# Kernel tuning notes

Measured on AMD Instinct MI355X. Metric: run time of the kernel, lower is better.

The kernel has to match this reference:

```python
import jax, jax.numpy as jnp
import numpy as np

B, N, D = 2, 2048, 1024
H = 16
DP = D // H          # projection dim per head = 64
SCALE = DP ** 0.5

def setup_inputs() -> dict:
    key = jax.random.key(0)
    ks = jax.random.split(key, 5)
    s_in = 1.0 / np.sqrt(D)
    s_merge = 1.0 / np.sqrt(H * DP)
    x = jax.random.normal(ks[0], (B, N, D), dtype=jnp.float32)
    W_qkv = jax.random.normal(ks[1], (D, 3 * H * DP), dtype=jnp.float32) * s_in
    b_qkv = jnp.zeros((3 * H * DP,), dtype=jnp.float32)
    W_out = jax.random.normal(ks[2], (H * DP, D), dtype=jnp.float32) * s_merge
    b_out = jnp.zeros((D,), dtype=jnp.float32)
    return {"x": x, "W_qkv": W_qkv, "b_qkv": b_qkv, "W_out": W_out, "b_out": b_out}

def reference(x, W_qkv, b_qkv, W_out, b_out):
    # packed QKV projection: (B,N,3*H*DP)
    qkv = jnp.einsum("bnd,de->bne", x, W_qkv) + b_qkv
    # reshape to (B,N,H,3*DP) -> (B,H,N,3*DP), split along last axis
    qkv = qkv.reshape(B, N, H, 3 * DP).transpose(0, 2, 1, 3)
    q, k, v = jnp.split(qkv, 3, axis=-1)                 # each (B,H,N,DP)
    scores = jnp.einsum("bhqd,bhkd->bhqk", q, k) / SCALE  # (B,H,N,N)
    attn = jax.nn.softmax(scores, axis=-1)
    out = jnp.einsum("bhqk,bhkd->bhqd", attn, v)          # (B,H,N,DP)
    out = out.transpose(0, 2, 1, 3).reshape(B, N, H * DP)
    return jnp.einsum("bne,ed->bnd", out, W_out) + b_out
```

## Files before the change

### kernel.cpp

```cpp
#include <hip/hip_runtime.h>
#include <hip/hip_bf16.h>

#define BB 2
#define NN 2048
#define DD 1024
#define HH 16
#define DP 64

typedef __attribute__((ext_vector_type(8))) short short8;
typedef __attribute__((ext_vector_type(4))) short short4v;
typedef __attribute__((ext_vector_type(4))) float float4v;
typedef __attribute__((ext_vector_type(16))) float f32x16;

static __device__ __forceinline__ short f2bf(float f) {
  union { float f; unsigned u; } v; v.f = f;
  unsigned r = v.u + 0x7fffu + ((v.u >> 16) & 1u);
  return (short)(r >> 16);
}

static __device__ __forceinline__ void gload16(const void* g, void* l) {
  __builtin_amdgcn_global_load_lds(
      (const __attribute__((address_space(1))) void*)g,
      (__attribute__((address_space(3))) void*)l, 16, 0, 0);
}

__global__ __launch_bounds__(256) void prep(
    const float* __restrict__ x, short* __restrict__ xb,
    const float* __restrict__ Wqkv, short* __restrict__ wqkt,
    const float* __restrict__ Wout, short* __restrict__ wott) {
  __shared__ short tile[32][33];
  const int b = blockIdx.x, t = threadIdx.x;
  if (b < 4096) {
    int i = (b * 256 + t) * 4;
    float4v f = *(const float4v*)(x + i);
    short4v s;
#pragma unroll
    for (int j = 0; j < 4; ++j) s[j] = f2bf(f[j]);
    *(short4v*)(xb + i) = s;
    return;
  }
  const float* in;  short* out;  int R, C, bx, by;
  if (b < 7168) { int idx = b - 4096; bx = idx % 96; by = idx / 96;
                  in = Wqkv; out = wqkt; R = 1024; C = 3072; }
  else          { int idx = b - 7168; bx = idx % 32; by = idx / 32;
                  in = Wout; out = wott; R = 1024; C = 1024; }
  int c0 = bx * 32, r0 = by * 32;
  int tx = t & 31, ty = t >> 5;
#pragma unroll
  for (int i = 0; i < 32; i += 8)
    tile[ty + i][tx] = f2bf(in[(size_t)(r0 + ty + i) * C + c0 + tx]);
  __syncthreads();
#pragma unroll
  for (int i = 0; i < 32; i += 8)
    out[(size_t)(c0 + ty + i) * R + r0 + tx] = tile[tx][ty + i];
}

__global__ __launch_bounds__(256, 6) void gemm_qkv_mfma(
    const short* __restrict__ A, const short* __restrict__ Bt,
    const float* __restrict__ bias,
    short* __restrict__ Qb, short* __restrict__ Kb, short* __restrict__ Vtb) {
  __shared__ short As[2][64 * 32];
  __shared__ short Bs[2][128 * 32];
  const int K = DD;
  const int t = threadIdx.x;
  const int w = t >> 6, lane = t & 63;
  const int l16 = lane & 15, quad = lane >> 4;
  const int wm = w >> 1, wn = w & 1;
  const int bm0 = blockIdx.y * 64;
  const int bn0 = blockIdx.x * 128;
  const int rA = lane >> 2, cA = lane & 3;
  const short* aRow  = A  + (size_t)(bm0 + w * 16 + rA) * K + cA * 8;
  const short* bRow0 = Bt + (size_t)(bn0 + w * 16 + rA) * K + cA * 8;
  const short* bRow1 = Bt + (size_t)(bn0 + 64 + w * 16 + rA) * K + cA * 8;
  char* AsB = (char*)&As[0][0] + w * 1024;
  char* BsB = (char*)&Bs[0][0] + w * 1024;
  float4v acc[2][4] = {};

  gload16(aRow, AsB);
  gload16(bRow0, BsB);
  gload16(bRow1, BsB + 4096);
  __syncthreads();

  int cur = 0;
  for (int k0 = 0; k0 < K; k0 += 32) {
    if (k0 + 32 < K) {
      const int nxt = cur ^ 1;
      gload16(aRow + k0 + 32, AsB + nxt * 4096);
      gload16(bRow0 + k0 + 32, BsB + nxt * 8192);
      gload16(bRow1 + k0 + 32, BsB + nxt * 8192 + 4096);
    }
    short8 af[2], bf[4];
#pragma unroll
    for (int mb = 0; mb < 2; ++mb)
      af[mb] = *(const short8*)&As[cur][((wm * 32 + mb * 16 + l16) * 4 + quad) * 8];
#pragma unroll
    for (int nb = 0; nb < 4; ++nb)
      bf[nb] = *(const short8*)&Bs[cur][((wn * 64 + nb * 16 + l16) * 4 + quad) * 8];
#pragma unroll
    for (int mb = 0; mb < 2; ++mb)
#pragma unroll
      for (int nb = 0; nb < 4; ++nb)
        acc[mb][nb] = __builtin_amdgcn_mfma_f32_16x16x32_bf16(af[mb], bf[nb],
                                                              acc[mb][nb], 0, 0, 0);
    __syncthreads();
    cur ^= 1;
  }

#pragma unroll
  for (int mb = 0; mb < 2; ++mb)
#pragma unroll
    for (int nb = 0; nb < 4; ++nb)
#pragma unroll
      for (int r = 0; r < 4; ++r) {
        int m = bm0 + wm * 32 + mb * 16 + quad * 4 + r;
        int e = bn0 + wn * 64 + nb * 16 + l16;
        float v = acc[mb][nb][r] + bias[e];
        int b_ = m >> 11;
        int n = m & 2047;
        int h = e / 192;
        int rr = e - h * 192;
        int which = rr >> 6;
        int d = rr & 63;
        if (which == 0)      Qb[((b_ * HH + h) * NN + n) * DP + d] = f2bf(v * 0.125f);
        else if (which == 1) Kb[((b_ * HH + h) * NN + n) * DP + d] = f2bf(v);
        else                 Vtb[((b_ * HH + h) * DP + d) * NN + n] = f2bf(v);
      }
}

__global__ __launch_bounds__(256, 4) void gemm_out_mfma(
    const short* __restrict__ A, const short* __restrict__ Bt,
    const float* __restrict__ bias, float* __restrict__ C) {
  __shared__ short As[2][64 * 32];
  __shared__ short Bs[2][64 * 32];
  const int K = DD;
  const int t = threadIdx.x;
  const int w = t >> 6, lane = t & 63;
  const int l16 = lane & 15, quad = lane >> 4;
  const int wm = w >> 1, wn = w & 1;
  const int bm0 = blockIdx.y * 64;
  const int bn0 = blockIdx.x * 64;
  const int rA = lane >> 2, cA = lane & 3;
  const short* aRow = A  + (size_t)(bm0 + w * 16 + rA) * K + cA * 8;
  const short* bRow = Bt + (size_t)(bn0 + w * 16 + rA) * K + cA * 8;
  char* AsB = (char*)&As[0][0] + w * 1024;
  char* BsB = (char*)&Bs[0][0] + w * 1024;
  float4v acc[2][2] = {};

  gload16(aRow, AsB);
  gload16(bRow, BsB);
  __syncthreads();

  int cur = 0;
  for (int k0 = 0; k0 < K; k0 += 32) {
    if (k0 + 32 < K) {
      const int nxt = cur ^ 1;
      gload16(aRow + k0 + 32, AsB + nxt * 4096);
      gload16(bRow + k0 + 32, BsB + nxt * 4096);
    }
    short8 af[2], bf[2];
#pragma unroll
    for (int mb = 0; mb < 2; ++mb)
      af[mb] = *(const short8*)&As[cur][((wm * 32 + mb * 16 + l16) * 4 + quad) * 8];
#pragma unroll
    for (int nb = 0; nb < 2; ++nb)
      bf[nb] = *(const short8*)&Bs[cur][((wn * 32 + nb * 16 + l16) * 4 + quad) * 8];
#pragma unroll
    for (int mb = 0; mb < 2; ++mb)
#pragma unroll
      for (int nb = 0; nb < 2; ++nb)
        acc[mb][nb] = __builtin_amdgcn_mfma_f32_16x16x32_bf16(af[mb], bf[nb],
                                                              acc[mb][nb], 0, 0, 0);
    __syncthreads();
    cur ^= 1;
  }

#pragma unroll
  for (int mb = 0; mb < 2; ++mb)
#pragma unroll
    for (int nb = 0; nb < 2; ++nb)
#pragma unroll
      for (int r = 0; r < 4; ++r) {
        int m = bm0 + wm * 32 + mb * 16 + quad * 4 + r;
        int e = bn0 + wn * 32 + nb * 16 + l16;
        C[(size_t)m * DD + e] = acc[mb][nb][r] + bias[e];
      }
}

#define FIXMAX 16.0f

__global__ __launch_bounds__(256, 2) void attn_mfma(
    const short* __restrict__ Qb, const short* __restrict__ Kb,
    const short* __restrict__ Vtb, short* __restrict__ Ob) {
  __shared__ short Ks[2][4096];
  __shared__ short Vs[2][4096];

  const int t = threadIdx.x;
  const int w = t >> 6;
  const int lane = t & 63;
  const int l31 = lane & 31;
  const int hi = lane >> 5;
  const int bh = blockIdx.y;
  const int q0 = blockIdx.x * 128 + w * 32;
  const size_t base  = (size_t)bh * NN * DP;
  const size_t baseT = (size_t)bh * DP * NN;

  short8 qf[4];
  {
    const short* qp = Qb + base + (size_t)(q0 + l31) * DP + hi * 8;
#pragma unroll
    for (int c = 0; c < 4; ++c) qf[c] = *(const short8*)(qp + c * 16);
  }

  f32x16 oacc[2] = {};
  float l_loc = 0.f;

  const int sRow = lane >> 3;
  const int sChk = (lane & 7) ^ sRow;
  const short* kSrc = Kb  + base  + (size_t)(w * 16 + sRow) * DP + sChk * 8;
  const short* vSrc = Vtb + baseT + (size_t)(w * 16 + sRow) * NN + sChk * 8;
  char* KsB = (char*)&Ks[0][0] + w * 2048;
  char* VsB = (char*)&Vs[0][0] + w * 2048;

  const int rswz = l31 & 7;
  int chs[4];
#pragma unroll
  for (int c = 0; c < 4; ++c) chs[c] = (((hi + 2 * c) ^ rswz) << 3);

  gload16(kSrc, KsB);
  gload16(kSrc + 8 * DP, KsB + 1024);
  gload16(vSrc, VsB);
  gload16(vSrc + 8 * NN, VsB + 1024);
  __syncthreads();

  for (int tt = 0; tt < NN / 64; ++tt) {
    const int buf = tt & 1;
    if (tt + 1 < NN / 64) {
      const int nxt = buf ^ 1;
      const int k1 = (tt + 1) * 64;
      gload16(kSrc + (size_t)k1 * DP, KsB + nxt * 8192);
      gload16(kSrc + (size_t)k1 * DP + 8 * DP, KsB + nxt * 8192 + 1024);
      gload16(vSrc + k1, VsB + nxt * 8192);
      gload16(vSrc + k1 + 8 * NN, VsB + nxt * 8192 + 1024);
    }
    const short* Kc = &Ks[buf][0];
    const short* Vc = &Vs[buf][0];

    short8 kf[2][4];
#pragma unroll
    for (int nb = 0; nb < 2; ++nb)
#pragma unroll
      for (int c = 0; c < 4; ++c)
        kf[nb][c] = *(const short8*)(Kc + (nb * 32 + l31) * 64 + chs[c]);

    f32x16 sacc[2] = {};
#pragma unroll
    for (int c = 0; c < 4; ++c) {
      sacc[0] = __builtin_amdgcn_mfma_f32_32x32x16_bf16(kf[0][c], qf[c], sacc[0], 0, 0, 0);
      sacc[1] = __builtin_amdgcn_mfma_f32_32x32x16_bf16(kf[1][c], qf[c], sacc[1], 0, 0, 0);
    }

    short8 vf[2][4];
#pragma unroll
    for (int db = 0; db < 2; ++db)
#pragma unroll
      for (int c = 0; c < 4; ++c)
        vf[db][c] = *(const short8*)(Vc + (db * 32 + l31) * 64 + chs[c]);

    short8 pb[4];
#pragma unroll
    for (int b = 0; b < 2; ++b) {
      float pe[16];
#pragma unroll
      for (int r = 0; r < 16; ++r) {
        pe[r] = __expf(sacc[b][r] - FIXMAX);
        l_loc += pe[r];
      }
      unsigned W[8];
#pragma unroll
      for (int j = 0; j < 8; ++j)
        asm("v_cvt_pk_bf16_f32 %0, %1, %2"
            : "=v"(W[j]) : "v"(pe[2 * j]), "v"(pe[2 * j + 1]));
      asm("v_permlane32_swap_b32 %0, %1" : "+v"(W[0]), "+v"(W[2]));
      asm("v_permlane32_swap_b32 %0, %1" : "+v"(W[1]), "+v"(W[3]));
      asm("v_permlane32_swap_b32 %0, %1" : "+v"(W[4]), "+v"(W[6]));
      asm("v_permlane32_swap_b32 %0, %1" : "+v"(W[5]), "+v"(W[7]));
      union { unsigned u[4]; short8 s; } f0, f1;
      f0.u[0] = W[0]; f0.u[1] = W[1]; f0.u[2] = W[2]; f0.u[3] = W[3];
      f1.u[0] = W[4]; f1.u[1] = W[5]; f1.u[2] = W[6]; f1.u[3] = W[7];
      pb[2 * b]     = f0.s;
      pb[2 * b + 1] = f1.s;
    }

#pragma unroll
    for (int c = 0; c < 4; ++c) {
      oacc[0] = __builtin_amdgcn_mfma_f32_32x32x16_bf16(vf[0][c], pb[c], oacc[0], 0, 0, 0);
      oacc[1] = __builtin_amdgcn_mfma_f32_32x32x16_bf16(vf[1][c], pb[c], oacc[1], 0, 0, 0);
    }

    __syncthreads();
  }

  const int b_ = bh >> 4, h = bh & 15;
  const float l_tot = l_loc + __shfl_xor(l_loc, 32);
  const float inv = 1.0f / l_tot;
  const int q = q0 + l31;
  short* orow = Ob + (size_t)(b_ * NN + q) * (HH * DP) + h * DP;
#pragma unroll
  for (int db = 0; db < 2; ++db)
#pragma unroll
    for (int g = 0; g < 4; ++g) {
      short4v s4;
#pragma unroll
      for (int e = 0; e < 4; ++e) s4[e] = f2bf(oacc[db][g * 4 + e] * inv);
      *(short4v*)(orow + db * 32 + g * 8 + hi * 4) = s4;
    }
}

extern "C" void kernel_launch(void* const* d_in, const int* in_sizes, int n_in,
                              void* d_out, int out_size, void* d_ws, size_t ws_size,
                              hipStream_t stream) {
  const float* x    = (const float*)d_in[0];
  const float* Wqkv = (const float*)d_in[1];
  const float* bqkv = (const float*)d_in[2];
  const float* Wout = (const float*)d_in[3];
  const float* bout = (const float*)d_in[4];
  float* out = (float*)d_out;

  const int nQKV = BB * HH * NN * DP;
  const int nX   = BB * NN * DD;
  short* qb   = (short*)d_ws;
  short* kb   = qb + nQKV;
  short* vtb  = kb + nQKV;
  short* ob   = vtb + nQKV;
  short* xb   = ob + nQKV;
  short* wqkt = xb + nX;
  short* wott = wqkt + 3 * HH * DP * DD;

  prep<<<4096 + 3072 + 1024, 256, 0, stream>>>(x, xb, Wqkv, wqkt, Wout, wott);

  gemm_qkv_mfma<<<dim3(3 * HH * DP / 128, BB * NN / 64), 256, 0, stream>>>(
      xb, wqkt, bqkv, qb, kb, vtb);
  attn_mfma<<<dim3(NN / 128, BB * HH), 256, 0, stream>>>(qb, kb, vtb, ob);
  gemm_out_mfma<<<dim3(DD / 64, BB * NN / 64), 256, 0, stream>>>(
      ob, wott, bout, out);
}
```

Before: 209.7 us.

## Enlarge QKV GEMM tile, halve attention block size, use exp2 softmax

The QKV GEMM block tile grows from 64x128 to 128x128, so each wave computes a 64x64 subtile and global loads are reused more, with fewer blocks and more accumulator registers. The attention kernel now runs 2 waves per 128-thread block covering 64 queries, which doubles the number of blocks, and each wave loads more of the K/V tile. The softmax exponent switches from __expf to a native exp2 by folding log2(e) into the Q scale and the fixed max offset. The costs are lower occupancy in the GEMM and more K/V reloads across attention blocks.

```diff
diff --git a/kernel.cpp b/kernel.cpp
--- a/kernel.cpp
+++ b/kernel.cpp
@@ -6,6 +6,8 @@
 #define DD 1024
 #define HH 16
 #define DP 64
+#define QSCALE 0.18033688f
+#define FIX2   23.08312065f
 
 typedef __attribute__((ext_vector_type(8))) short short8;
 typedef __attribute__((ext_vector_type(4))) short short4v;
@@ -55,49 +57,50 @@
     out[(size_t)(c0 + ty + i) * R + r0 + tx] = tile[tx][ty + i];
 }
 
-__global__ __launch_bounds__(256, 6) void gemm_qkv_mfma(
+__global__ __launch_bounds__(256, 3) void gemm_qkv_mfma(
     const short* __restrict__ A, const short* __restrict__ Bt,
     const float* __restrict__ bias,
     short* __restrict__ Qb, short* __restrict__ Kb, short* __restrict__ Vtb) {
-  __shared__ short As[2][64 * 32];
+  __shared__ short As[2][128 * 32];
   __shared__ short Bs[2][128 * 32];
   const int K = DD;
   const int t = threadIdx.x;
   const int w = t >> 6, lane = t & 63;
   const int l16 = lane & 15, quad = lane >> 4;
   const int wm = w >> 1, wn = w & 1;
-  const int bm0 = blockIdx.y * 64;
+  const int bm0 = blockIdx.y * 128;
   const int bn0 = blockIdx.x * 128;
   const int rA = lane >> 2, cA = lane & 3;
-  const short* aRow  = A  + (size_t)(bm0 + w * 16 + rA) * K + cA * 8;
-  const short* bRow0 = Bt + (size_t)(bn0 + w * 16 + rA) * K + cA * 8;
-  const short* bRow1 = Bt + (size_t)(bn0 + 64 + w * 16 + rA) * K + cA * 8;
-  char* AsB = (char*)&As[0][0] + w * 1024;
-  char* BsB = (char*)&Bs[0][0] + w * 1024;
-  float4v acc[2][4] = {};
+  const short* aRow = A  + (size_t)(bm0 + w * 32 + rA) * K + cA * 8;
+  const short* bRow = Bt + (size_t)(bn0 + w * 32 + rA) * K + cA * 8;
+  char* AsB = (char*)&As[0][0] + w * 2048;
+  char* BsB = (char*)&Bs[0][0] + w * 2048;
+  float4v acc[4][4] = {};
 
   gload16(aRow, AsB);
-  gload16(bRow0, BsB);
-  gload16(bRow1, BsB + 4096);
+  gload16(aRow + 16 * K, AsB + 1024);
+  gload16(bRow, BsB);
+  gload16(bRow + 16 * K, BsB + 1024);
   __syncthreads();
 
   int cur = 0;
   for (int k0 = 0; k0 < K; k0 += 32) {
     if (k0 + 32 < K) {
       const int nxt = cur ^ 1;
-      gload16(aRow + k0 + 32, AsB + nxt * 4096);
-      gload16(bRow0 + k0 + 32, BsB + nxt * 8192);
-      gload16(bRow1 + k0 + 32, BsB + nxt * 8192 + 4096);
-    }
-    short8 af[2], bf[4];
-#pragma unroll
-    for (int mb = 0; mb < 2; ++mb)
-      af[mb] = *(const short8*)&As[cur][((wm * 32 + mb * 16 + l16) * 4 + quad) * 8];
+      gload16(aRow + k0 + 32, AsB + nxt * 8192);
+      gload16(aRow + 16 * K + k0 + 32, AsB + nxt * 8192 + 1024);
+      gload16(bRow + k0 + 32, BsB + nxt * 8192);
+      gload16(bRow + 16 * K + k0 + 32, BsB + nxt * 8192 + 1024);
+    }
+    short8 af[4], bf[4];
+#pragma unroll
+    for (int mb = 0; mb < 4; ++mb)
+      af[mb] = *(const short8*)&As[cur][((wm * 64 + mb * 16 + l16) * 4 + quad) * 8];
 #pragma unroll
     for (int nb = 0; nb < 4; ++nb)
       bf[nb] = *(const short8*)&Bs[cur][((wn * 64 + nb * 16 + l16) * 4 + quad) * 8];
 #pragma unroll
-    for (int mb = 0; mb < 2; ++mb)
+    for (int mb = 0; mb < 4; ++mb)
 #pragma unroll
       for (int nb = 0; nb < 4; ++nb)
         acc[mb][nb] = __builtin_amdgcn_mfma_f32_16x16x32_bf16(af[mb], bf[nb],
@@ -107,12 +110,12 @@
   }
 
 #pragma unroll
-  for (int mb = 0; mb < 2; ++mb)
+  for (int mb = 0; mb < 4; ++mb)
 #pragma unroll
     for (int nb = 0; nb < 4; ++nb)
 #pragma unroll
       for (int r = 0; r < 4; ++r) {
-        int m = bm0 + wm * 32 + mb * 16 + quad * 4 + r;
+        int m = bm0 + wm * 64 + mb * 16 + quad * 4 + r;
         int e = bn0 + wn * 64 + nb * 16 + l16;
         float v = acc[mb][nb][r] + bias[e];
         int b_ = m >> 11;
@@ -121,7 +124,7 @@
         int rr = e - h * 192;
         int which = rr >> 6;
         int d = rr & 63;
-        if (which == 0)      Qb[((b_ * HH + h) * NN + n) * DP + d] = f2bf(v * 0.125f);
+        if (which == 0)      Qb[((b_ * HH + h) * NN + n) * DP + d] = f2bf(v * QSCALE);
         else if (which == 1) Kb[((b_ * HH + h) * NN + n) * DP + d] = f2bf(v);
         else                 Vtb[((b_ * HH + h) * DP + d) * NN + n] = f2bf(v);
       }
@@ -186,9 +189,7 @@
       }
 }
 
-#define FIXMAX 16.0f
-
-__global__ __launch_bounds__(256, 2) void attn_mfma(
+__global__ __launch_bounds__(128, 2) void attn_mfma(
     const short* __restrict__ Qb, const short* __restrict__ Kb,
     const short* __restrict__ Vtb, short* __restrict__ Ob) {
   __shared__ short Ks[2][4096];
@@ -200,7 +201,7 @@
   const int l31 = lane & 31;
   const int hi = lane >> 5;
   const int bh = blockIdx.y;
-  const int q0 = blockIdx.x * 128 + w * 32;
+  const int q0 = blockIdx.x * 64 + w * 32;
   const size_t base  = (size_t)bh * NN * DP;
   const size_t baseT = (size_t)bh * DP * NN;
 
@@ -216,20 +217,21 @@
 
   const int sRow = lane >> 3;
   const int sChk = (lane & 7) ^ sRow;
-  const short* kSrc = Kb  + base  + (size_t)(w * 16 + sRow) * DP + sChk * 8;
-  const short* vSrc = Vtb + baseT + (size_t)(w * 16 + sRow) * NN + sChk * 8;
-  char* KsB = (char*)&Ks[0][0] + w * 2048;
-  char* VsB = (char*)&Vs[0][0] + w * 2048;
+  const short* kSrc = Kb  + base  + (size_t)(w * 32 + sRow) * DP + sChk * 8;
+  const short* vSrc = Vtb + baseT + (size_t)(w * 32 + sRow) * NN + sChk * 8;
+  char* KsB = (char*)&Ks[0][0] + w * 4096;
+  char* VsB = (char*)&Vs[0][0] + w * 4096;
 
   const int rswz = l31 & 7;
   int chs[4];
 #pragma unroll
   for (int c = 0; c < 4; ++c) chs[c] = (((hi + 2 * c) ^ rswz) << 3);
 
-  gload16(kSrc, KsB);
-  gload16(kSrc + 8 * DP, KsB + 1024);
-  gload16(vSrc, VsB);
-  gload16(vSrc + 8 * NN, VsB + 1024);
+#pragma unroll
+  for (int g = 0; g < 4; ++g) {
+    gload16(kSrc + (size_t)g * 8 * DP, KsB + g * 1024);
+    gload16(vSrc + (size_t)g * 8 * NN, VsB + g * 1024);
+  }
   __syncthreads();
 
   for (int tt = 0; tt < NN / 64; ++tt) {
@@ -237,10 +239,11 @@
     if (tt + 1 < NN / 64) {
       const int nxt = buf ^ 1;
       const int k1 = (tt + 1) * 64;
-      gload16(kSrc + (size_t)k1 * DP, KsB + nxt * 8192);
-      gload16(kSrc + (size_t)k1 * DP + 8 * DP, KsB + nxt * 8192 + 1024);
-      gload16(vSrc + k1, VsB + nxt * 8192);
-      gload16(vSrc + k1 + 8 * NN, VsB + nxt * 8192 + 1024);
+#pragma unroll
+      for (int g = 0; g < 4; ++g) {
+        gload16(kSrc + (size_t)(k1 + g * 8) * DP, KsB + nxt * 8192 + g * 1024);
+        gload16(vSrc + (size_t)g * 8 * NN + k1, VsB + nxt * 8192 + g * 1024);
+      }
     }
     const short* Kc = &Ks[buf][0];
     const short* Vc = &Vs[buf][0];
@@ -272,7 +275,7 @@
       float pe[16];
 #pragma unroll
       for (int r = 0; r < 16; ++r) {
-        pe[r] = __expf(sacc[b][r] - FIXMAX);
+        pe[r] = __builtin_amdgcn_exp2f(sacc[b][r] - FIX2);
         l_loc += pe[r];
       }
       unsigned W[8];
@@ -338,9 +341,9 @@
 
   prep<<<4096 + 3072 + 1024, 256, 0, stream>>>(x, xb, Wqkv, wqkt, Wout, wott);
 
-  gemm_qkv_mfma<<<dim3(3 * HH * DP / 128, BB * NN / 64), 256, 0, stream>>>(
+  gemm_qkv_mfma<<<dim3(3 * HH * DP / 128, BB * NN / 128), 256, 0, stream>>>(
       xb, wqkt, bqkv, qb, kb, vtb);
-  attn_mfma<<<dim3(NN / 128, BB * HH), 256, 0, stream>>>(qb, kb, vtb, ob);
+  attn_mfma<<<dim3(NN / 64, BB * HH), 128, 0, stream>>>(qb, kb, vtb, ob);
   gemm_out_mfma<<<dim3(DD / 64, BB * NN / 64), 256, 0, stream>>>(
       ob, wott, bout, out);
 }
```

New measurement: 204.8 us. 2.3% less time.
